# Kernel tuning notes

Hardware: AMD Instinct MI355X
Metric: run time of the kernel (lower is better)

Reference implementation:

```python
import jax, jax.numpy as jnp
import numpy as np

B, M, IN, HID, A = 4096, 64, 3, 128, 64
D = 50.0                       # waveguide_bound
H_CONST = 5.0
PMAX = 10.0 ** (30 / 10 - 3)   # = 1.0 (30 dBm in Watts)
C_LIGHT = 3.0e8
FC = 6.0e9
DELTA_MIN = (C_LIGHT / FC) / 2.0  # 0.025
ALPHA = 0.2                    # LeakyReLU slope


def setup_inputs() -> dict:
    key = jax.random.key(0)
    ks = jax.random.split(key, 9)
    s = lambda k, sh: (jax.random.normal(k, sh, jnp.float32) * 0.1)
    return {
        "users": jax.random.normal(ks[0], (B, M, IN), jnp.float32),
        "W1": s(ks[1], (IN, HID)),    # GAT layer 1 projection (applied as h @ W)
        "a1": s(ks[2], (2 * HID,)),   # GAT layer 1 attention vector
        "W2": s(ks[3], (HID, HID)),   # GAT layer 2 projection
        "a2": s(ks[4], (2 * HID,)),
        "mw1": s(ks[5], (HID, 32)),   # MLP Linear(hidden, 32)
        "mb1": jnp.zeros((32,), jnp.float32),
        "mw2": s(ks[6], (32, 2 * A)), # MLP Linear(32, 2*num_antennas)
        "mb2": jnp.zeros((2 * A,), jnp.float32),
    }


def gat_layer(h, W, a):
    # Wh: [B, M, d]
    Wh = h @ W
    d = W.shape[1]
    # e[b,i,j] = leakyrelu( cat(Wh_i, Wh_j) . a ) = leakyrelu( Wh_i.a[:d] + Wh_j.a[d:] )
    si = Wh @ a[:d]          # [B, M]
    sj = Wh @ a[d:]          # [B, M]
    e = jax.nn.leaky_relu(si[:, :, None] + sj[:, None, :], ALPHA)  # [B, M, M]
    attn = jax.nn.softmax(e, axis=-1)  # softmax over neighbors j (dropout p=0 -> identity)
    h_prime = jnp.einsum('bij,bjd->bid', attn, Wh)
    return jax.nn.elu(h_prime)


def reference(users, W1, a1, W2, a2, mw1, mb1, mw2, mb2):
    h = gat_layer(users, W1, a1)
    h = gat_layer(h, W2, a2)
    pooled = jnp.max(h, axis=1)                      # [B, hidden]
    readout = jax.nn.relu(pooled @ mw1 + mb1) @ mw2 + mb2  # [B, 2A]
    raw_delta, raw_power = readout[:, :A], readout[:, A:]
    eps = 1e-6
    raw_delta = jax.nn.relu(raw_delta) + eps
    raw_power = jax.nn.relu(raw_power) + eps
    Bmax = 2.0 * D - (A - 1) * DELTA_MIN
    delta = Bmax * raw_delta / (jnp.sum(raw_delta, axis=1, keepdims=True) + eps)
    power = PMAX * raw_power / (jnp.sum(raw_power, axis=1, keepdims=True) + eps)
    return power, delta
```

## Files before the change

kernel.cpp:

```cpp
#include <hip/hip_runtime.h>

#define NBATCH 4096
#define OUT2 (NBATCH * 64)

typedef _Float16 f16;
typedef __attribute__((ext_vector_type(8))) _Float16 f16x8;
typedef __attribute__((ext_vector_type(4))) _Float16 f16x4;
typedef __attribute__((ext_vector_type(4))) float f32x4;

__device__ __forceinline__ float lrelu(float x) { return x > 0.0f ? x : 0.2f * x; }
__device__ __forceinline__ float elu1(float x)  { return x > 0.0f ? x : __expf(x) - 1.0f; }

__global__ void prep(const float* __restrict__ W2, const float* __restrict__ W1,
                     const float* __restrict__ a1, const float* __restrict__ a2,
                     f16* __restrict__ w2b, float* __restrict__ w1a, f16* __restrict__ w2ab) {
    const int flat = blockIdx.x * 256 + threadIdx.x;
    const int slot = flat >> 3, j = flat & 7;
    const int F2T = slot >> 8, kf = (slot >> 6) & 3, ln = slot & 63;
    const int lq = ln >> 4, lr = ln & 15;
    w2b[flat] = (f16)W2[(kf * 32 + lq * 8 + j) * 128 + F2T * 16 + lr];
    if (flat < 2048) {
        const int ks = flat >> 9, ln2 = (flat >> 3) & 63, jj = flat & 7;
        const int k = ks * 32 + ((ln2 >> 4) & 3) * 8 + jj;
        const int n = ln2 & 15;
        float v = 0.f;
        if (n < 2) {
            const float* av = a2 + n * 128;
            for (int f2 = 0; f2 < 128; ++f2) v = fmaf(W2[k * 128 + f2], av[f2], v);
        }
        w2ab[flat] = (f16)v;
    }
    if (flat >= 16381) {
        const int c = flat - 16381;
        float si = 0.f, sj = 0.f;
        for (int f = 0; f < 128; ++f) {
            const float w = W1[c * 128 + f];
            si = fmaf(w, a1[f], si);
            sj = fmaf(w, a1[128 + f], sj);
        }
        w1a[c] = si; w1a[3 + c] = sj;
    }
}

__global__ __launch_bounds__(64, 2)
void gat_kernel(const float* __restrict__ users,
                const float* __restrict__ W1,
                const f16* __restrict__ w2b,
                const float* __restrict__ w1a,
                const f16* __restrict__ w2ab,
                const float* __restrict__ mw1,
                const float* __restrict__ mb1,
                const float* __restrict__ mw2,
                const float* __restrict__ mb2,
                float* __restrict__ out)
{
    const int b0 = blockIdx.x * 2;
    const int lane = threadIdx.x;
    const int lr = lane & 15;
    const int lq = lane >> 4;

    __shared__ __align__(16) char smem[18688];
    f16*   sMain = (f16*)smem;
    float* sSiA  = (float*)(smem + 16384);
    float* sSjA  = (float*)(smem + 16896);
    float* sPoolA= (float*)(smem + 17408);
    float* sHidA = (float*)(smem + 18432);

    #pragma unroll
    for (int g = 0; g < 2; ++g) {
        const float* u = users + (b0 + g) * 192;
        const float x = u[lane * 3], y = u[lane * 3 + 1], z = u[lane * 3 + 2];
        sSiA[g * 64 + lane] = fmaf(x, w1a[0], fmaf(y, w1a[1], z * w1a[2]));
        sSjA[g * 64 + lane] = fmaf(x, w1a[3], fmaf(y, w1a[4], z * w1a[5]));
    }
    __syncthreads();

    f16x8 bfr[2][4];
    float inv1[2][4];
    #pragma unroll
    for (int g = 0; g < 2; ++g) {
        const float* sSi = sSiA + g * 64;
        const float* sSj = sSjA + g * 64;
        float sjv[16];
        *(float4*)&sjv[0]  = *(const float4*)&sSj[lq * 8];
        *(float4*)&sjv[4]  = *(const float4*)&sSj[lq * 8 + 4];
        *(float4*)&sjv[8]  = *(const float4*)&sSj[32 + lq * 8];
        *(float4*)&sjv[12] = *(const float4*)&sSj[32 + lq * 8 + 4];
        f16x8 ap[4][2];
        #pragma unroll
        for (int mt = 0; mt < 4; ++mt) {
            const float si = sSi[mt * 16 + lr];
            float lsum = 0.f;
            #pragma unroll
            for (int jj = 0; jj < 8; ++jj) {
                float p = __expf(lrelu(si + sjv[jj]));
                f16 ph = (f16)p; lsum += (float)ph; ap[mt][0][jj] = ph;
                p = __expf(lrelu(si + sjv[8 + jj]));
                ph = (f16)p; lsum += (float)ph; ap[mt][1][jj] = ph;
            }
            lsum += __shfl_xor(lsum, 16, 64);
            lsum += __shfl_xor(lsum, 32, 64);
            inv1[g][mt] = 1.0f / lsum;
        }
        f16x8 af2[2];
        #pragma unroll
        for (int ks = 0; ks < 2; ++ks) {
            #pragma unroll
            for (int jj = 0; jj < 8; ++jj) {
                const int node = ks * 32 + lq * 8 + jj;
                af2[ks][jj] = (lr < 3) ? (f16)users[(b0 + g) * 192 + node * 3 + lr] : (f16)0.f;
            }
        }
        #pragma unroll
        for (int nt = 0; nt < 4; ++nt) {
            f32x4 d1 = (f32x4){0.f, 0.f, 0.f, 0.f};
            d1 = __builtin_amdgcn_mfma_f32_16x16x32_f16(af2[0], ap[nt][0], d1, 0, 0, 0);
            d1 = __builtin_amdgcn_mfma_f32_16x16x32_f16(af2[1], ap[nt][1], d1, 0, 0, 0);
            const float c0 = __shfl(d1[0], lr, 64);
            const float c1 = __shfl(d1[1], lr, 64);
            const float c2 = __shfl(d1[2], lr, 64);
            #pragma unroll
            for (int jj = 0; jj < 8; ++jj) bfr[g][nt][jj] = (f16)0.f;
            if (lq == 0) {
                bfr[g][nt][0] = (f16)c0; bfr[g][nt][1] = (f16)c1; bfr[g][nt][2] = (f16)c2;
            }
        }
    }

    f16x8 hf[2][4][4];
    #pragma unroll
    for (int h = 0; h < 2; ++h) {
        __syncthreads();
        #pragma unroll
        for (int ftl = 0; ftl < 4; ++ftl) {
            f16x8 af3;
            #pragma unroll
            for (int jj = 0; jj < 8; ++jj) af3[jj] = (f16)0.f;
            if (lq == 0) {
                #pragma unroll
                for (int jj = 0; jj < 3; ++jj)
                    af3[jj] = (f16)W1[jj * 128 + (h * 4 + ftl) * 16 + lr];
            }
            #pragma unroll
            for (int g = 0; g < 2; ++g) {
                #pragma unroll
                for (int nt = 0; nt < 4; ++nt) {
                    f32x4 acc = (f32x4){0.f, 0.f, 0.f, 0.f};
                    acc = __builtin_amdgcn_mfma_f32_16x16x32_f16(af3, bfr[g][nt], acc, 0, 0, 0);
                    f16x4 hv;
                    #pragma unroll
                    for (int r = 0; r < 4; ++r) hv[r] = (f16)elu1(acc[r] * inv1[g][nt]);
                    const int n = nt * 16 + lr;
                    const int gg = 2 * ftl + (lq >> 1);
                    *(f16x4*)&sMain[g * 4096 + n * 64 + ((gg ^ (n & 7)) << 3) + ((lq & 1) * 4)] = hv;
                }
            }
        }
        __syncthreads();
        #pragma unroll
        for (int g = 0; g < 2; ++g) {
            #pragma unroll
            for (int nt = 0; nt < 4; ++nt) {
                const int n = nt * 16 + lr;
                #pragma unroll
                for (int ksl = 0; ksl < 2; ++ksl)
                    hf[g][nt][h * 2 + ksl] =
                        *(const f16x8*)&sMain[g * 4096 + n * 64 + (((ksl * 4 + lq) ^ (n & 7)) << 3)];
            }
        }
    }

    {
        f32x4 sacc[2][4];
        #pragma unroll
        for (int g = 0; g < 2; ++g)
            #pragma unroll
            for (int mt = 0; mt < 4; ++mt) sacc[g][mt] = (f32x4){0.f, 0.f, 0.f, 0.f};
        #pragma unroll
        for (int ks = 0; ks < 4; ++ks) {
            f16x8 bsw = *(const f16x8*)(w2ab + (ks * 64 + lane) * 8);
            #pragma unroll
            for (int g = 0; g < 2; ++g)
                #pragma unroll
                for (int mt = 0; mt < 4; ++mt)
                    sacc[g][mt] = __builtin_amdgcn_mfma_f32_16x16x32_f16(hf[g][mt][ks], bsw, sacc[g][mt], 0, 0, 0);
        }
        if (lr < 2) {
            #pragma unroll
            for (int g = 0; g < 2; ++g) {
                float* dst = (lr == 0) ? (sSiA + g * 64) : (sSjA + g * 64);
                #pragma unroll
                for (int mt = 0; mt < 4; ++mt)
                    #pragma unroll
                    for (int r = 0; r < 4; ++r)
                        dst[mt * 16 + lq * 4 + r] = sacc[g][mt][r];
            }
        }
    }

    #pragma unroll
    for (int g = 0; g < 2; ++g) {
        __syncthreads();
        #pragma unroll
        for (int h = 0; h < 2; ++h) {
            #pragma unroll
            for (int f2t = 0; f2t < 4; ++f2t) {
                f16x8 bw2[4];
                #pragma unroll
                for (int kf = 0; kf < 4; ++kf)
                    bw2[kf] = *(const f16x8*)(w2b + (((h * 4 + f2t) * 4 + kf) * 64 + lane) * 8);
                #pragma unroll
                for (int ntile = 0; ntile < 4; ++ntile) {
                    f32x4 acc = (f32x4){0.f, 0.f, 0.f, 0.f};
                    #pragma unroll
                    for (int kf = 0; kf < 4; ++kf)
                        acc = __builtin_amdgcn_mfma_f32_16x16x32_f16(hf[g][ntile][kf], bw2[kf], acc, 0, 0, 0);
                    const int fl = h * 64 + f2t * 16 + lr;
                    const int gg = ntile * 2 + (lq >> 1);
                    f16x4 hv;
                    #pragma unroll
                    for (int r = 0; r < 4; ++r) hv[r] = (f16)acc[r];
                    *(f16x4*)&sMain[fl * 64 + ((gg ^ (fl & 7)) << 3) + ((lq & 1) * 4)] = hv;
                }
            }
        }
        __syncthreads();

        const float* sSi = sSiA + g * 64;
        const float* sSj = sSjA + g * 64;
        f16x8 bp[4][2];
        float inv2[4];
        {
            float sjv[16];
            *(float4*)&sjv[0]  = *(const float4*)&sSj[lq * 8];
            *(float4*)&sjv[4]  = *(const float4*)&sSj[lq * 8 + 4];
            *(float4*)&sjv[8]  = *(const float4*)&sSj[32 + lq * 8];
            *(float4*)&sjv[12] = *(const float4*)&sSj[32 + lq * 8 + 4];
            #pragma unroll
            for (int mt = 0; mt < 4; ++mt) {
                const float si = sSi[mt * 16 + lr];
                float lsum = 0.f;
                #pragma unroll
                for (int jj = 0; jj < 8; ++jj) {
                    float p = __expf(lrelu(si + sjv[jj]));
                    f16 ph = (f16)p; lsum += (float)ph; bp[mt][0][jj] = ph;
                    p = __expf(lrelu(si + sjv[8 + jj]));
                    ph = (f16)p; lsum += (float)ph; bp[mt][1][jj] = ph;
                }
                lsum += __shfl_xor(lsum, 16, 64);
                lsum += __shfl_xor(lsum, 32, 64);
                inv2[mt] = 1.0f / lsum;
            }
        }
        #pragma unroll
        for (int ftl = 0; ftl < 8; ++ftl) {
            const int fl = ftl * 16 + lr;
            f16x8 bh0 = *(const f16x8*)&sMain[fl * 64 + ((lq ^ (fl & 7)) << 3)];
            f16x8 bh1 = *(const f16x8*)&sMain[fl * 64 + (((4 + lq) ^ (fl & 7)) << 3)];
            f32x4 mx4 = (f32x4){-1e30f, -1e30f, -1e30f, -1e30f};
            #pragma unroll
            for (int mt = 0; mt < 4; ++mt) {
                f32x4 acc = (f32x4){0.f, 0.f, 0.f, 0.f};
                acc = __builtin_amdgcn_mfma_f32_16x16x32_f16(bh0, bp[mt][0], acc, 0, 0, 0);
                acc = __builtin_amdgcn_mfma_f32_16x16x32_f16(bh1, bp[mt][1], acc, 0, 0, 0);
                #pragma unroll
                for (int r = 0; r < 4; ++r)
                    mx4[r] = fmaxf(mx4[r], acc[r] * inv2[mt]);
            }
            #pragma unroll
            for (int m = 1; m < 16; m <<= 1) {
                #pragma unroll
                for (int r = 0; r < 4; ++r)
                    mx4[r] = fmaxf(mx4[r], __shfl_xor(mx4[r], m, 64));
            }
            if (lr == 0) {
                float4 pv;
                pv.x = elu1(mx4[0]); pv.y = elu1(mx4[1]);
                pv.z = elu1(mx4[2]); pv.w = elu1(mx4[3]);
                *(float4*)&sPoolA[g * 128 + ftl * 16 + lq * 4] = pv;
            }
        }
    }
    __syncthreads();

    {
        const int o = lane & 31, hh = lane >> 5;
        float s0 = 0.f, s1 = 0.f;
        #pragma unroll 8
        for (int kk = 0; kk < 64; ++kk) {
            const int c = hh * 64 + kk;
            const float w = mw1[c * 32 + o];
            s0 = fmaf(sPoolA[c], w, s0);
            s1 = fmaf(sPoolA[128 + c], w, s1);
        }
        s0 += __shfl_xor(s0, 32, 64);
        s1 += __shfl_xor(s1, 32, 64);
        const float bb = mb1[o];
        if (lane < 32) {
            sHidA[lane] = fmaxf(s0 + bb, 0.0f);
            sHidA[32 + lane] = fmaxf(s1 + bb, 0.0f);
        }
    }
    __syncthreads();
    {
        const float mbA = mb2[lane], mbB = mb2[64 + lane];
        float sA0 = mbA, sB0 = mbB, sA1 = mbA, sB1 = mbB;
        #pragma unroll 8
        for (int q = 0; q < 32; ++q) {
            const float wA = mw2[q * 128 + lane];
            const float wB = mw2[q * 128 + 64 + lane];
            const float h0 = sHidA[q], h1 = sHidA[32 + q];
            sA0 = fmaf(h0, wA, sA0);  sB0 = fmaf(h0, wB, sB0);
            sA1 = fmaf(h1, wA, sA1);  sB1 = fmaf(h1, wB, sB1);
        }
        float rA0 = fmaxf(sA0, 0.0f) + 1e-6f, rB0 = fmaxf(sB0, 0.0f) + 1e-6f;
        float rA1 = fmaxf(sA1, 0.0f) + 1e-6f, rB1 = fmaxf(sB1, 0.0f) + 1e-6f;
        float uA0 = rA0, uB0 = rB0, uA1 = rA1, uB1 = rB1;
        #pragma unroll
        for (int m = 1; m < 64; m <<= 1) {
            uA0 += __shfl_xor(uA0, m, 64);  uB0 += __shfl_xor(uB0, m, 64);
            uA1 += __shfl_xor(uA1, m, 64);  uB1 += __shfl_xor(uB1, m, 64);
        }
        out[b0 * 64 + lane]              = rB0 / (uB0 + 1e-6f);
        out[OUT2 + b0 * 64 + lane]       = 98.425f * rA0 / (uA0 + 1e-6f);
        out[(b0 + 1) * 64 + lane]        = rB1 / (uB1 + 1e-6f);
        out[OUT2 + (b0 + 1) * 64 + lane] = 98.425f * rA1 / (uA1 + 1e-6f);
    }
}

extern "C" void kernel_launch(void* const* d_in, const int* in_sizes, int n_in,
                              void* d_out, int out_size, void* d_ws, size_t ws_size,
                              hipStream_t stream) {
    const float* users = (const float*)d_in[0];
    const float* W1    = (const float*)d_in[1];
    const float* a1    = (const float*)d_in[2];
    const float* W2    = (const float*)d_in[3];
    const float* a2    = (const float*)d_in[4];
    const float* mw1   = (const float*)d_in[5];
    const float* mb1   = (const float*)d_in[6];
    const float* mw2   = (const float*)d_in[7];
    const float* mb2   = (const float*)d_in[8];
    float* out = (float*)d_out;

    f16*   w2b  = (f16*)d_ws;
    float* w1a  = (float*)((char*)d_ws + 32768);
    f16*   w2ab = (f16*)((char*)d_ws + 32800);

    prep<<<64, 256, 0, stream>>>(W2, W1, a1, a2, w2b, w1a, w2ab);
    gat_kernel<<<NBATCH / 2, 64, 0, stream>>>(users, W1, w2b, w1a, w2ab,
                                              mw1, mb1, mw2, mb2, out);
}
```

Before: 113.7 us.

## Process one batch per workgroup and stream layer-2 projection per feature tile

Each single-wave workgroup now handles one batch element instead of two. This halves register and LDS use and raises the launch-bounds occupancy hint from 2 to 4. The layer-2 projection and attention aggregation are restructured into a non-unrolled loop over 8 feature tiles that reuses a small 16-row LDS buffer. The aim is more resident waves to hide latency, at the cost of twice as many workgroups, repeated weight loads per batch, and an extra barrier per tile.

```diff
diff --git a/kernel.cpp b/kernel.cpp
--- a/kernel.cpp
+++ b/kernel.cpp
@@ -42,7 +42,7 @@
     }
 }
 
-__global__ __launch_bounds__(64, 2)
+__global__ __launch_bounds__(64, 4)
 void gat_kernel(const float* __restrict__ users,
                 const float* __restrict__ W1,
                 const f16* __restrict__ w2b,
@@ -54,33 +54,30 @@
                 const float* __restrict__ mb2,
                 float* __restrict__ out)
 {
-    const int b0 = blockIdx.x * 2;
+    const int b = blockIdx.x;
     const int lane = threadIdx.x;
     const int lr = lane & 15;
     const int lq = lane >> 4;
 
-    __shared__ __align__(16) char smem[18688];
+    __shared__ __align__(16) char smem[9344];
     f16*   sMain = (f16*)smem;
-    float* sSiA  = (float*)(smem + 16384);
-    float* sSjA  = (float*)(smem + 16896);
-    float* sPoolA= (float*)(smem + 17408);
-    float* sHidA = (float*)(smem + 18432);
-
-    #pragma unroll
-    for (int g = 0; g < 2; ++g) {
-        const float* u = users + (b0 + g) * 192;
+    float* sSi   = (float*)(smem + 8192);
+    float* sSj   = (float*)(smem + 8448);
+    float* sPool = (float*)(smem + 8704);
+    float* sHid  = (float*)(smem + 9216);
+
+    const float* u = users + b * 192;
+
+    {
         const float x = u[lane * 3], y = u[lane * 3 + 1], z = u[lane * 3 + 2];
-        sSiA[g * 64 + lane] = fmaf(x, w1a[0], fmaf(y, w1a[1], z * w1a[2]));
-        sSjA[g * 64 + lane] = fmaf(x, w1a[3], fmaf(y, w1a[4], z * w1a[5]));
+        sSi[lane] = fmaf(x, w1a[0], fmaf(y, w1a[1], z * w1a[2]));
+        sSj[lane] = fmaf(x, w1a[3], fmaf(y, w1a[4], z * w1a[5]));
     }
     __syncthreads();
 
-    f16x8 bfr[2][4];
-    float inv1[2][4];
-    #pragma unroll
-    for (int g = 0; g < 2; ++g) {
-        const float* sSi = sSiA + g * 64;
-        const float* sSj = sSjA + g * 64;
+    f16x8 bfr[4];
+    float inv1[4];
+    {
         float sjv[16];
         *(float4*)&sjv[0]  = *(const float4*)&sSj[lq * 8];
         *(float4*)&sjv[4]  = *(const float4*)&sSj[lq * 8 + 4];
@@ -100,7 +97,7 @@
             }
             lsum += __shfl_xor(lsum, 16, 64);
             lsum += __shfl_xor(lsum, 32, 64);
-            inv1[g][mt] = 1.0f / lsum;
+            inv1[mt] = 1.0f / lsum;
         }
         f16x8 af2[2];
         #pragma unroll
@@ -108,7 +105,7 @@
             #pragma unroll
             for (int jj = 0; jj < 8; ++jj) {
                 const int node = ks * 32 + lq * 8 + jj;
-                af2[ks][jj] = (lr < 3) ? (f16)users[(b0 + g) * 192 + node * 3 + lr] : (f16)0.f;
+                af2[ks][jj] = (lr < 3) ? (f16)u[node * 3 + lr] : (f16)0.f;
             }
         }
         #pragma unroll
@@ -120,14 +117,14 @@
             const float c1 = __shfl(d1[1], lr, 64);
             const float c2 = __shfl(d1[2], lr, 64);
             #pragma unroll
-            for (int jj = 0; jj < 8; ++jj) bfr[g][nt][jj] = (f16)0.f;
+            for (int jj = 0; jj < 8; ++jj) bfr[nt][jj] = (f16)0.f;
             if (lq == 0) {
-                bfr[g][nt][0] = (f16)c0; bfr[g][nt][1] = (f16)c1; bfr[g][nt][2] = (f16)c2;
-            }
-        }
-    }
-
-    f16x8 hf[2][4][4];
+                bfr[nt][0] = (f16)c0; bfr[nt][1] = (f16)c1; bfr[nt][2] = (f16)c2;
+            }
+        }
+    }
+
+    f16x8 hf[4][4];
     #pragma unroll
     for (int h = 0; h < 2; ++h) {
         __syncthreads();
@@ -142,189 +139,152 @@
                     af3[jj] = (f16)W1[jj * 128 + (h * 4 + ftl) * 16 + lr];
             }
             #pragma unroll
-            for (int g = 0; g < 2; ++g) {
+            for (int nt = 0; nt < 4; ++nt) {
+                f32x4 acc = (f32x4){0.f, 0.f, 0.f, 0.f};
+                acc = __builtin_amdgcn_mfma_f32_16x16x32_f16(af3, bfr[nt], acc, 0, 0, 0);
+                f16x4 hv;
                 #pragma unroll
-                for (int nt = 0; nt < 4; ++nt) {
-                    f32x4 acc = (f32x4){0.f, 0.f, 0.f, 0.f};
-                    acc = __builtin_amdgcn_mfma_f32_16x16x32_f16(af3, bfr[g][nt], acc, 0, 0, 0);
-                    f16x4 hv;
-                    #pragma unroll
-                    for (int r = 0; r < 4; ++r) hv[r] = (f16)elu1(acc[r] * inv1[g][nt]);
-                    const int n = nt * 16 + lr;
-                    const int gg = 2 * ftl + (lq >> 1);
-                    *(f16x4*)&sMain[g * 4096 + n * 64 + ((gg ^ (n & 7)) << 3) + ((lq & 1) * 4)] = hv;
-                }
-            }
-        }
-        __syncthreads();
-        #pragma unroll
-        for (int g = 0; g < 2; ++g) {
-            #pragma unroll
-            for (int nt = 0; nt < 4; ++nt) {
+                for (int r = 0; r < 4; ++r) hv[r] = (f16)elu1(acc[r] * inv1[nt]);
                 const int n = nt * 16 + lr;
-                #pragma unroll
-                for (int ksl = 0; ksl < 2; ++ksl)
-                    hf[g][nt][h * 2 + ksl] =
-                        *(const f16x8*)&sMain[g * 4096 + n * 64 + (((ksl * 4 + lq) ^ (n & 7)) << 3)];
-            }
-        }
-    }
-
-    {
-        f32x4 sacc[2][4];
-        #pragma unroll
-        for (int g = 0; g < 2; ++g)
-            #pragma unroll
-            for (int mt = 0; mt < 4; ++mt) sacc[g][mt] = (f32x4){0.f, 0.f, 0.f, 0.f};
+                const int gg = 2 * ftl + (lq >> 1);
+                *(f16x4*)&sMain[n * 64 + ((gg ^ (n & 7)) << 3) + ((lq & 1) * 4)] = hv;
+            }
+        }
+        __syncthreads();
+        #pragma unroll
+        for (int nt = 0; nt < 4; ++nt) {
+            const int n = nt * 16 + lr;
+            #pragma unroll
+            for (int ksl = 0; ksl < 2; ++ksl)
+                hf[nt][h * 2 + ksl] =
+                    *(const f16x8*)&sMain[n * 64 + (((ksl * 4 + lq) ^ (n & 7)) << 3)];
+        }
+    }
+
+    {
+        f32x4 sacc[4];
+        #pragma unroll
+        for (int mt = 0; mt < 4; ++mt) sacc[mt] = (f32x4){0.f, 0.f, 0.f, 0.f};
         #pragma unroll
         for (int ks = 0; ks < 4; ++ks) {
             f16x8 bsw = *(const f16x8*)(w2ab + (ks * 64 + lane) * 8);
             #pragma unroll
-            for (int g = 0; g < 2; ++g)
-                #pragma unroll
-                for (int mt = 0; mt < 4; ++mt)
-                    sacc[g][mt] = __builtin_amdgcn_mfma_f32_16x16x32_f16(hf[g][mt][ks], bsw, sacc[g][mt], 0, 0, 0);
-        }
+            for (int mt = 0; mt < 4; ++mt)
+                sacc[mt] = __builtin_amdgcn_mfma_f32_16x16x32_f16(hf[mt][ks], bsw, sacc[mt], 0, 0, 0);
+        }
+        __syncthreads();
         if (lr < 2) {
-            #pragma unroll
-            for (int g = 0; g < 2; ++g) {
-                float* dst = (lr == 0) ? (sSiA + g * 64) : (sSjA + g * 64);
-                #pragma unroll
-                for (int mt = 0; mt < 4; ++mt)
-                    #pragma unroll
-                    for (int r = 0; r < 4; ++r)
-                        dst[mt * 16 + lq * 4 + r] = sacc[g][mt][r];
-            }
-        }
-    }
-
-    #pragma unroll
-    for (int g = 0; g < 2; ++g) {
-        __syncthreads();
-        #pragma unroll
-        for (int h = 0; h < 2; ++h) {
-            #pragma unroll
-            for (int f2t = 0; f2t < 4; ++f2t) {
-                f16x8 bw2[4];
-                #pragma unroll
-                for (int kf = 0; kf < 4; ++kf)
-                    bw2[kf] = *(const f16x8*)(w2b + (((h * 4 + f2t) * 4 + kf) * 64 + lane) * 8);
-                #pragma unroll
-                for (int ntile = 0; ntile < 4; ++ntile) {
-                    f32x4 acc = (f32x4){0.f, 0.f, 0.f, 0.f};
-                    #pragma unroll
-                    for (int kf = 0; kf < 4; ++kf)
-                        acc = __builtin_amdgcn_mfma_f32_16x16x32_f16(hf[g][ntile][kf], bw2[kf], acc, 0, 0, 0);
-                    const int fl = h * 64 + f2t * 16 + lr;
-                    const int gg = ntile * 2 + (lq >> 1);
-                    f16x4 hv;
-                    #pragma unroll
-                    for (int r = 0; r < 4; ++r) hv[r] = (f16)acc[r];
-                    *(f16x4*)&sMain[fl * 64 + ((gg ^ (fl & 7)) << 3) + ((lq & 1) * 4)] = hv;
-                }
-            }
-        }
-        __syncthreads();
-
-        const float* sSi = sSiA + g * 64;
-        const float* sSj = sSjA + g * 64;
-        f16x8 bp[4][2];
-        float inv2[4];
-        {
-            float sjv[16];
-            *(float4*)&sjv[0]  = *(const float4*)&sSj[lq * 8];
-            *(float4*)&sjv[4]  = *(const float4*)&sSj[lq * 8 + 4];
-            *(float4*)&sjv[8]  = *(const float4*)&sSj[32 + lq * 8];
-            *(float4*)&sjv[12] = *(const float4*)&sSj[32 + lq * 8 + 4];
-            #pragma unroll
-            for (int mt = 0; mt < 4; ++mt) {
-                const float si = sSi[mt * 16 + lr];
-                float lsum = 0.f;
-                #pragma unroll
-                for (int jj = 0; jj < 8; ++jj) {
-                    float p = __expf(lrelu(si + sjv[jj]));
-                    f16 ph = (f16)p; lsum += (float)ph; bp[mt][0][jj] = ph;
-                    p = __expf(lrelu(si + sjv[8 + jj]));
-                    ph = (f16)p; lsum += (float)ph; bp[mt][1][jj] = ph;
-                }
-                lsum += __shfl_xor(lsum, 16, 64);
-                lsum += __shfl_xor(lsum, 32, 64);
-                inv2[mt] = 1.0f / lsum;
-            }
-        }
-        #pragma unroll
-        for (int ftl = 0; ftl < 8; ++ftl) {
-            const int fl = ftl * 16 + lr;
-            f16x8 bh0 = *(const f16x8*)&sMain[fl * 64 + ((lq ^ (fl & 7)) << 3)];
-            f16x8 bh1 = *(const f16x8*)&sMain[fl * 64 + (((4 + lq) ^ (fl & 7)) << 3)];
-            f32x4 mx4 = (f32x4){-1e30f, -1e30f, -1e30f, -1e30f};
-            #pragma unroll
-            for (int mt = 0; mt < 4; ++mt) {
-                f32x4 acc = (f32x4){0.f, 0.f, 0.f, 0.f};
-                acc = __builtin_amdgcn_mfma_f32_16x16x32_f16(bh0, bp[mt][0], acc, 0, 0, 0);
-                acc = __builtin_amdgcn_mfma_f32_16x16x32_f16(bh1, bp[mt][1], acc, 0, 0, 0);
+            float* dst = (lr == 0) ? sSi : sSj;
+            #pragma unroll
+            for (int mt = 0; mt < 4; ++mt)
                 #pragma unroll
                 for (int r = 0; r < 4; ++r)
-                    mx4[r] = fmaxf(mx4[r], acc[r] * inv2[mt]);
-            }
-            #pragma unroll
-            for (int m = 1; m < 16; m <<= 1) {
-                #pragma unroll
-                for (int r = 0; r < 4; ++r)
-                    mx4[r] = fmaxf(mx4[r], __shfl_xor(mx4[r], m, 64));
-            }
-            if (lr == 0) {
-                float4 pv;
-                pv.x = elu1(mx4[0]); pv.y = elu1(mx4[1]);
-                pv.z = elu1(mx4[2]); pv.w = elu1(mx4[3]);
-                *(float4*)&sPoolA[g * 128 + ftl * 16 + lq * 4] = pv;
-            }
+                    dst[mt * 16 + lq * 4 + r] = sacc[mt][r];
         }
     }
     __syncthreads();
 
+    f16x8 bp[4][2];
+    float inv2[4];
+    {
+        float sjv[16];
+        *(float4*)&sjv[0]  = *(const float4*)&sSj[lq * 8];
+        *(float4*)&sjv[4]  = *(const float4*)&sSj[lq * 8 + 4];
+        *(float4*)&sjv[8]  = *(const float4*)&sSj[32 + lq * 8];
+        *(float4*)&sjv[12] = *(const float4*)&sSj[32 + lq * 8 + 4];
+        #pragma unroll
+        for (int mt = 0; mt < 4; ++mt) {
+            const float si = sSi[mt * 16 + lr];
+            float lsum = 0.f;
+            #pragma unroll
+            for (int jj = 0; jj < 8; ++jj) {
+                float p = __expf(lrelu(si + sjv[jj]));
+                f16 ph = (f16)p; lsum += (float)ph; bp[mt][0][jj] = ph;
+                p = __expf(lrelu(si + sjv[8 + jj]));
+                ph = (f16)p; lsum += (float)ph; bp[mt][1][jj] = ph;
+            }
+            lsum += __shfl_xor(lsum, 16, 64);
+            lsum += __shfl_xor(lsum, 32, 64);
+            inv2[mt] = 1.0f / lsum;
+        }
+    }
+
+    #pragma unroll 1
+    for (int ft = 0; ft < 8; ++ft) {
+        f16x8 bw2[4];
+        #pragma unroll
+        for (int kf = 0; kf < 4; ++kf)
+            bw2[kf] = *(const f16x8*)(w2b + ((ft * 4 + kf) * 64 + lane) * 8);
+        #pragma unroll
+        for (int nt = 0; nt < 4; ++nt) {
+            f32x4 acc = (f32x4){0.f, 0.f, 0.f, 0.f};
+            #pragma unroll
+            for (int kf = 0; kf < 4; ++kf)
+                acc = __builtin_amdgcn_mfma_f32_16x16x32_f16(hf[nt][kf], bw2[kf], acc, 0, 0, 0);
+            const int gg = nt * 2 + (lq >> 1);
+            f16x4 hv;
+            #pragma unroll
+            for (int r = 0; r < 4; ++r) hv[r] = (f16)acc[r];
+            *(f16x4*)&sMain[lr * 64 + ((gg ^ (lr & 7)) << 3) + ((lq & 1) * 4)] = hv;
+        }
+        __syncthreads();
+
+        f16x8 bh0 = *(const f16x8*)&sMain[lr * 64 + ((lq ^ (lr & 7)) << 3)];
+        f16x8 bh1 = *(const f16x8*)&sMain[lr * 64 + (((4 + lq) ^ (lr & 7)) << 3)];
+        f32x4 mx4 = (f32x4){-1e30f, -1e30f, -1e30f, -1e30f};
+        #pragma unroll
+        for (int mt = 0; mt < 4; ++mt) {
+            f32x4 acc = (f32x4){0.f, 0.f, 0.f, 0.f};
+            acc = __builtin_amdgcn_mfma_f32_16x16x32_f16(bh0, bp[mt][0], acc, 0, 0, 0);
+            acc = __builtin_amdgcn_mfma_f32_16x16x32_f16(bh1, bp[mt][1], acc, 0, 0, 0);
+            #pragma unroll
+            for (int r = 0; r < 4; ++r)
+                mx4[r] = fmaxf(mx4[r], acc[r] * inv2[mt]);
+        }
+        #pragma unroll
+        for (int m = 1; m < 16; m <<= 1) {
+            #pragma unroll
+            for (int r = 0; r < 4; ++r)
+                mx4[r] = fmaxf(mx4[r], __shfl_xor(mx4[r], m, 64));
+        }
+        if (lr == 0) {
+            float4 pv;
+            pv.x = elu1(mx4[0]); pv.y = elu1(mx4[1]);
+            pv.z = elu1(mx4[2]); pv.w = elu1(mx4[3]);
+            *(float4*)&sPool[ft * 16 + lq * 4] = pv;
+        }
+        __syncthreads();
+    }
+
     {
         const int o = lane & 31, hh = lane >> 5;
-        float s0 = 0.f, s1 = 0.f;
+        float s0 = 0.f;
         #pragma unroll 8
         for (int kk = 0; kk < 64; ++kk) {
             const int c = hh * 64 + kk;
-            const float w = mw1[c * 32 + o];
-            s0 = fmaf(sPoolA[c], w, s0);
-            s1 = fmaf(sPoolA[128 + c], w, s1);
+            s0 = fmaf(sPool[c], mw1[c * 32 + o], s0);
         }
         s0 += __shfl_xor(s0, 32, 64);
-        s1 += __shfl_xor(s1, 32, 64);
-        const float bb = mb1[o];
-        if (lane < 32) {
-            sHidA[lane] = fmaxf(s0 + bb, 0.0f);
-            sHidA[32 + lane] = fmaxf(s1 + bb, 0.0f);
-        }
+        if (lane < 32) sHid[lane] = fmaxf(s0 + mb1[o], 0.0f);
     }
     __syncthreads();
     {
-        const float mbA = mb2[lane], mbB = mb2[64 + lane];
-        float sA0 = mbA, sB0 = mbB, sA1 = mbA, sB1 = mbB;
+        float sA = mb2[lane], sB = mb2[64 + lane];
         #pragma unroll 8
         for (int q = 0; q < 32; ++q) {
             const float wA = mw2[q * 128 + lane];
             const float wB = mw2[q * 128 + 64 + lane];
-            const float h0 = sHidA[q], h1 = sHidA[32 + q];
-            sA0 = fmaf(h0, wA, sA0);  sB0 = fmaf(h0, wB, sB0);
-            sA1 = fmaf(h1, wA, sA1);  sB1 = fmaf(h1, wB, sB1);
-        }
-        float rA0 = fmaxf(sA0, 0.0f) + 1e-6f, rB0 = fmaxf(sB0, 0.0f) + 1e-6f;
-        float rA1 = fmaxf(sA1, 0.0f) + 1e-6f, rB1 = fmaxf(sB1, 0.0f) + 1e-6f;
-        float uA0 = rA0, uB0 = rB0, uA1 = rA1, uB1 = rB1;
+            const float h0 = sHid[q];
+            sA = fmaf(h0, wA, sA);  sB = fmaf(h0, wB, sB);
+        }
+        float rA = fmaxf(sA, 0.0f) + 1e-6f, rB = fmaxf(sB, 0.0f) + 1e-6f;
+        float uA = rA, uB = rB;
         #pragma unroll
         for (int m = 1; m < 64; m <<= 1) {
-            uA0 += __shfl_xor(uA0, m, 64);  uB0 += __shfl_xor(uB0, m, 64);
-            uA1 += __shfl_xor(uA1, m, 64);  uB1 += __shfl_xor(uB1, m, 64);
-        }
-        out[b0 * 64 + lane]              = rB0 / (uB0 + 1e-6f);
-        out[OUT2 + b0 * 64 + lane]       = 98.425f * rA0 / (uA0 + 1e-6f);
-        out[(b0 + 1) * 64 + lane]        = rB1 / (uB1 + 1e-6f);
-        out[OUT2 + (b0 + 1) * 64 + lane] = 98.425f * rA1 / (uA1 + 1e-6f);
+            uA += __shfl_xor(uA, m, 64);  uB += __shfl_xor(uB, m, 64);
+        }
+        out[b * 64 + lane]        = rB / (uB + 1e-6f);
+        out[OUT2 + b * 64 + lane] = 98.425f * rA / (uA + 1e-6f);
     }
 }
 
@@ -347,6 +307,6 @@
     f16*   w2ab = (f16*)((char*)d_ws + 32800);
 
     prep<<<64, 256, 0, stream>>>(W2, W1, a1, a2, w2b, w1a, w2ab);
-    gat_kernel<<<NBATCH / 2, 64, 0, stream>>>(users, W1, w2b, w1a, w2ab,
-                                              mw1, mb1, mw2, mb2, out);
+    gat_kernel<<<NBATCH, 64, 0, stream>>>(users, W1, w2b, w1a, w2ab,
+                                          mw1, mb1, mw2, mb2, out);
 }
```

Result: slower. 128.4 us (+13.0%).
